# Kernel optimization log

Measured on AMD Instinct MI355X. Metric: run time of the kernel, lower is better.

Reference implementation:

```python
import jax, jax.numpy as jnp
import numpy as np

NH, DH, DHR = 16, 128, 64  # heads, head dim, decoupled rope dim
ROPE_BASE = 10000.0

def _rope(x):
    # x: (B, L, H, Dr) with Dr even; interleaved-pair RoPE (torchtune style)
    B, L, H, Dr = x.shape
    pos = jnp.arange(L, dtype=jnp.float32)
    inv_freq = 1.0 / (ROPE_BASE ** (jnp.arange(0, Dr, 2, dtype=jnp.float32) / Dr))
    ang = pos[:, None] * inv_freq[None, :]          # (L, Dr/2)
    cos = jnp.cos(ang)[None, :, None, :].astype(x.dtype)
    sin = jnp.sin(ang)[None, :, None, :].astype(x.dtype)
    x1, x2 = x[..., 0::2], x[..., 1::2]
    out = jnp.stack([x1 * cos - x2 * sin, x1 * sin + x2 * cos], axis=-1)
    return out.reshape(B, L, H, Dr)

def setup_inputs() -> dict:
    key = jax.random.key(0)
    ks = jax.random.split(key, 9)
    s = 0.02
    return {
        'x':     jax.random.normal(ks[0], (2, 2048, 2048), jnp.float32),
        'W_DKV': jax.random.normal(ks[1], (2048, 682), jnp.float32) * s,
        'W_UK':  jax.random.normal(ks[2], (682, 2048), jnp.float32) * s,
        'W_UV':  jax.random.normal(ks[3], (682, 2048), jnp.float32) * s,
        'W_KR':  jax.random.normal(ks[4], (2048, 64), jnp.float32) * s,
        'W_DQ':  jax.random.normal(ks[5], (2048, 682), jnp.float32) * s,
        'W_UQ':  jax.random.normal(ks[6], (682, 2048), jnp.float32) * s,
        'W_QR':  jax.random.normal(ks[7], (682, 1024), jnp.float32) * s,
        'W_O':   jax.random.normal(ks[8], (2048, 2048), jnp.float32) * s,
    }

def reference(x, W_DKV, W_UK, W_UV, W_KR, W_DQ, W_UQ, W_QR, W_O):
    B, L, D = x.shape
    # --- KV path ---
    c_KV = x @ W_DKV                                   # (B, L, dc)
    k_C = (c_KV @ W_UK).reshape(B, L, NH, DH)          # content keys
    k_R = _rope((x @ W_KR).reshape(B, L, 1, DHR))      # shared rope key head
    k_R = jnp.broadcast_to(k_R, (B, L, NH, DHR))
    k = jnp.concatenate([k_C, k_R], axis=-1)           # (B, L, NH, DH+DHR)
    v = (c_KV @ W_UV).reshape(B, L, NH, DH)
    # --- Q path ---
    c_Q = x @ W_DQ                                     # (B, L, dc')
    q_C = (c_Q @ W_UQ).reshape(B, L, NH, DH)
    q_R = _rope((c_Q @ W_QR).reshape(B, L, NH, DHR))
    q = jnp.concatenate([q_C, q_R], axis=-1)           # (B, L, NH, DH+DHR)
    # --- attention (causal) ---
    scale = 1.0 / jnp.sqrt(jnp.float32(DH + DHR))
    scores = jnp.einsum('blhd,bmhd->bhlm', q, k) * scale
    causal = jnp.tril(jnp.ones((L, L), dtype=bool))
    scores = jnp.where(causal[None, None], scores, jnp.finfo(scores.dtype).min)
    attn = jax.nn.softmax(scores, axis=-1)
    o = jnp.einsum('bhlm,bmhd->blhd', attn, v).reshape(B, L, NH * DH)
    return o @ W_O
```

## Files before the change

kernel.cpp:

```cpp
#include <hip/hip_runtime.h>
#include <stdint.h>

typedef __attribute__((ext_vector_type(8))) __bf16 bf16x8;
typedef __attribute__((ext_vector_type(4))) float f32x4;

#define DEVI static __device__ __forceinline__

DEVI uint16_t f2b(float f) {
  uint32_t u = __float_as_uint(f);
  u += 0x7FFFu + ((u >> 16) & 1u);
  return (uint16_t)(u >> 16);
}
DEVI float b2f(uint16_t b) { return __uint_as_float(((uint32_t)b) << 16); }

DEVI void gl_lds16(const void* g, void* l) {
  __builtin_amdgcn_global_load_lds((const __attribute__((address_space(1))) void*)g,
                                   (__attribute__((address_space(3))) void*)l, 16, 0, 0);
}

DEVI f32x4 mfma16(bf16x8 a, bf16x8 b, f32x4 c) {
  return __builtin_amdgcn_mfma_f32_16x16x32_bf16(a, b, c, 0, 0, 0);
}

#define BARX asm volatile("s_barrier" ::: "memory")
#define WLG0 asm volatile("s_waitcnt lgkmcnt(0)" ::: "memory")
#define WV4 asm volatile("s_waitcnt vmcnt(4)" ::: "memory")
#define PRIO1 __builtin_amdgcn_s_setprio(1)
#define PRIO0 __builtin_amdgcn_s_setprio(0)

static constexpr size_t OFF_XB = 0;
static constexpr size_t OFF_WD = 8388608;
static constexpr size_t OFF_WUKV = OFF_WD + 3670016;
static constexpr size_t OFF_WUQR = OFF_WUKV + 3145728;
static constexpr size_t OFF_WO = OFF_WUQR + 2359296;
static constexpr size_t OFF_CD = OFF_WO + 4194304;
static constexpr size_t OFF_CUKV = OFF_CD + 7340032;
static constexpr size_t OFF_CUQR = OFF_CUKV + 16777216;
static constexpr size_t OFF_VT = OFF_CUQR + 12582912;

__global__ void pre_kernel(const float* __restrict__ x, const float* __restrict__ Wdkv,
                           const float* __restrict__ Wuk, const float* __restrict__ Wuv,
                           const float* __restrict__ Wkr, const float* __restrict__ Wdq,
                           const float* __restrict__ Wuq, const float* __restrict__ Wqr,
                           const float* __restrict__ Wo, uint16_t* __restrict__ ws) {
  const int bid = blockIdx.x;
  const int t = threadIdx.x;
  if (bid >= 3264) {
    int id = (bid - 3264) * 256 + t;
    float4 v = ((const float4*)x)[id];
    uint16_t o[4] = {f2b(v.x), f2b(v.y), f2b(v.z), f2b(v.w)};
    *(uint64_t*)&ws[OFF_XB + (size_t)id * 4] = *(uint64_t*)o;
    return;
  }
  const float* W;
  uint16_t* Wt;
  int Kw, Nw, Kp, nx, rb;
  if (bid < 384) {
    W = Wdkv; Wt = ws + OFF_WD; Kw = 2048; Nw = 682; Kp = 2048; nx = 12; rb = bid;
  } else if (bid < 768) {
    W = Wdq; Wt = ws + OFF_WD + (size_t)768 * 2048; Kw = 2048; Nw = 682; Kp = 2048; nx = 12; rb = bid - 384;
  } else if (bid < 896) {
    W = Wkr; Wt = ws + OFF_WD + (size_t)1536 * 2048; Kw = 2048; Nw = 64; Kp = 2048; nx = 4; rb = bid - 768;
  } else if (bid < 1280) {
    W = Wuk; Wt = ws + OFF_WUKV; Kw = 682; Nw = 2048; Kp = 768; nx = 32; rb = bid - 896;
  } else if (bid < 1664) {
    W = Wuv; Wt = ws + OFF_WUKV + (size_t)2048 * 768; Kw = 682; Nw = 2048; Kp = 768; nx = 32; rb = bid - 1280;
  } else if (bid < 2048) {
    W = Wuq; Wt = ws + OFF_WUQR; Kw = 682; Nw = 2048; Kp = 768; nx = 32; rb = bid - 1664;
  } else if (bid < 2240) {
    W = Wqr; Wt = ws + OFF_WUQR + (size_t)2048 * 768; Kw = 682; Nw = 1024; Kp = 768; nx = 16; rb = bid - 2048;
  } else {
    W = Wo; Wt = ws + OFF_WO; Kw = 2048; Nw = 2048; Kp = 2048; nx = 32; rb = bid - 2240;
  }
  const int n0 = (rb % nx) * 64, k0 = (rb / nx) * 64;
  __shared__ uint16_t T[64][72];
#pragma unroll
  for (int p = 0; p < 2; ++p) {
    int r = p * 32 + (t >> 3);
    int c0 = (t & 7) * 8;
    int gr = k0 + r;
#pragma unroll
    for (int e = 0; e < 8; ++e) {
      int gc = n0 + c0 + e;
      float v = (gr < Kw && gc < Nw) ? W[(size_t)gr * Nw + gc] : 0.f;
      T[c0 + e][r] = f2b(v);
    }
  }
  __syncthreads();
#pragma unroll
  for (int p = 0; p < 2; ++p) {
    int dr = p * 32 + (t >> 3);
    int mc = (t & 7) * 8;
    uint16_t tmp[8];
#pragma unroll
    for (int e = 0; e < 8; ++e) tmp[e] = T[dr][mc + e];
    *(uint64_t*)&Wt[(size_t)(n0 + dr) * Kp + k0 + mc] = ((uint64_t*)tmp)[0];
    *(uint64_t*)&Wt[(size_t)(n0 + dr) * Kp + k0 + mc + 4] = ((uint64_t*)tmp)[1];
  }
}

template <int BM, bool F32OUT>
__global__ __launch_bounds__(512, 2) void gemm8(const uint16_t* __restrict__ A, int lda,
                                                const uint16_t* __restrict__ Bt,
                                                void* __restrict__ Cv, int ldc, int K) {
  constexpr int MF = BM / 32;
  constexpr int MH = MF / 2;
  constexpr int AL = BM / 128;
  constexpr int ABYTES = BM * 128;
  __shared__ char lds[2 * BM * 128 + 2 * 256 * 128];
  char* const LB = lds + 2 * ABYTES;
  const int tid = threadIdx.x;
  const int lane = tid & 63;
  const int lr = lane & 15, lgb = (lane >> 4) * 16;
  const int wid = tid >> 6;
  const int g = wid >> 2;
  const int wc = (wid & 3) * 64;
  const int rA0 = g * (BM / 2) + lr;
  const int rB0 = wc + lr;
  const size_t row0 = (size_t)blockIdx.y * BM, col0 = (size_t)blockIdx.x * 256;
  const char* Agb = (const char*)(A + row0 * lda);
  const char* Btb = (const char*)(Bt + col0 * K);
  const size_t ldab = (size_t)lda * 2;
  const size_t ldbb = (size_t)K * 2;
  const int nk = K >> 6;
  const int ni = nk >> 1;

  f32x4 acc[MF][4] = {};
  bf16x8 aF[MH][2], bF[4][2];

  auto stageA = [&](int kt, int buf, int hf) {
#pragma unroll
    for (int j = 0; j < AL; ++j) {
      int c = j * 512 + tid;
      int cl = c ^ (((c >> 5) & 1) << 1);
      int row = hf * (BM / 2) + (cl >> 3);
      gl_lds16(Agb + (size_t)row * ldab + (size_t)kt * 128 + (cl & 7) * 16,
               lds + buf * ABYTES + hf * (ABYTES / 2) + (j * 512 + (tid & 0x1C0)) * 16);
    }
  };
  auto stageB = [&](int kt, int buf, int hf) {
#pragma unroll
    for (int j = 0; j < 2; ++j) {
      int c = j * 512 + tid;
      int cl = c ^ (((c >> 5) & 1) << 1);
      int row = hf * 128 + (cl >> 3);
      gl_lds16(Btb + (size_t)row * ldbb + (size_t)kt * 128 + (cl & 7) * 16,
               LB + buf * 32768 + hf * 16384 + (j * 512 + (tid & 0x1C0)) * 16);
    }
  };
  auto ldAm = [&](int buf, int mb) {
#pragma unroll
    for (int m = 0; m < MH; ++m) {
      int r = rA0 + (mb + m) * 16;
      int ro = r * 128;
      int sw = ((r >> 2) & 1) << 5;
#pragma unroll
      for (int kk = 0; kk < 2; ++kk)
        aF[m][kk] = *(const bf16x8*)(lds + buf * ABYTES + ((ro + kk * 64 + lgb) ^ sw));
    }
  };
  auto ldBn = [&](int buf, int nb) {
#pragma unroll
    for (int n = 0; n < 2; ++n) {
      int r = rB0 + (nb + n) * 16;
      int ro = r * 128;
      int sw = ((r >> 2) & 1) << 5;
#pragma unroll
      for (int kk = 0; kk < 2; ++kk)
        bF[nb + n][kk] = *(const bf16x8*)(LB + buf * 32768 + ((ro + kk * 64 + lgb) ^ sw));
    }
  };
  auto mmac = [&](int mb, int nb) {
#pragma unroll
    for (int m = 0; m < MH; ++m)
#pragma unroll
      for (int n = 0; n < 2; ++n)
#pragma unroll
        for (int kk = 0; kk < 2; ++kk)
          acc[mb + m][nb + n] = mfma16(aF[m][kk], bF[nb + n][kk], acc[mb + m][nb + n]);
  };

  stageA(0, 0, 0); stageA(0, 0, 1); stageB(0, 0, 0); stageB(0, 0, 1);
  stageB(1, 1, 0); stageB(1, 1, 1);
  WV4; BARX;

  for (int i = 0; i < ni; ++i) {
    const int t1 = 2 * i + 1;
    const int tn = (2 * i + 2 < nk) ? 2 * i + 2 : nk - 1;
    const int tn1 = (2 * i + 3 < nk) ? 2 * i + 3 : nk - 1;
    ldAm(0, 0); ldBn(0, 0); stageA(t1, 1, 0);
    BARX; WLG0; PRIO1; mmac(0, 0); PRIO0; BARX;
    ldBn(0, 2); stageA(t1, 1, 1);
    BARX; WLG0; PRIO1; mmac(0, 2); PRIO0; BARX;
    ldAm(0, MH); stageB(tn, 0, 0);
    BARX; WLG0; PRIO1; mmac(MH, 0); PRIO0; BARX;
    stageB(tn, 0, 1);
    BARX; PRIO1; mmac(MH, 2); PRIO0; WV4; BARX;
    ldAm(1, 0); ldBn(1, 0); stageA(tn, 0, 0);
    BARX; WLG0; PRIO1; mmac(0, 0); PRIO0; BARX;
    ldBn(1, 2); stageA(tn, 0, 1);
    BARX; WLG0; PRIO1; mmac(0, 2); PRIO0; BARX;
    ldAm(1, MH); stageB(tn1, 1, 0);
    BARX; WLG0; PRIO1; mmac(MH, 0); PRIO0; BARX;
    stageB(tn1, 1, 1);
    BARX; PRIO1; mmac(MH, 2); PRIO0; WV4; BARX;
  }
  asm volatile("s_waitcnt vmcnt(0)" ::: "memory");

#pragma unroll
  for (int m = 0; m < MF; ++m)
#pragma unroll
    for (int n = 0; n < 4; ++n)
#pragma unroll
      for (int j = 0; j < 4; ++j) {
        size_t row = row0 + g * (BM / 2) + m * 16 + (lane >> 4) * 4 + j;
        size_t col = col0 + wc + n * 16 + lr;
        if (F32OUT)
          ((float*)Cv)[row * ldc + col] = acc[m][n][j];
        else
          ((uint16_t*)Cv)[row * ldc + col] = f2b(acc[m][n][j]);
      }
}

template <bool F32OUT>
__global__ __launch_bounds__(512, 2) void gemm4p(const uint16_t* __restrict__ A, int lda,
                                                 const uint16_t* __restrict__ Bt,
                                                 void* __restrict__ Cv, int ldc, int K) {
  constexpr int ABYTES = 128 * 128;
  __shared__ char lds[2 * ABYTES + 2 * 32768];
  char* const LB = lds + 2 * ABYTES;
  const int tid = threadIdx.x;
  const int lane = tid & 63;
  const int lr = lane & 15, lgb = (lane >> 4) * 16;
  const int wid = tid >> 6;
  const int g = wid >> 2;
  const int wc = (wid & 3) * 64;
  const int rA0 = g * 64 + lr;
  const int rB0 = wc + lr;
  const size_t row0 = (size_t)blockIdx.y * 128, col0 = (size_t)blockIdx.x * 256;
  const char* Agb = (const char*)(A + row0 * lda);
  const char* Btb = (const char*)(Bt + col0 * K);
  const size_t ldab = (size_t)lda * 2;
  const size_t ldbb = (size_t)K * 2;
  const int nk = K >> 6;
  const int ni = nk >> 1;

  f32x4 acc[4][4] = {};
  bf16x8 aF[2][2], bF[4][2];

  auto stageA = [&](int kt, int buf) {
#pragma unroll
    for (int j = 0; j < 2; ++j) {
      int c = j * 512 + tid;
      int cl = c ^ (((c >> 5) & 1) << 1);
      gl_lds16(Agb + (size_t)(cl >> 3) * ldab + (size_t)kt * 128 + (cl & 7) * 16,
               lds + buf * ABYTES + (j * 512 + (tid & 0x1C0)) * 16);
    }
  };
  auto stageBfull = [&](int kt, int buf) {
#pragma unroll
    for (int j = 0; j < 4; ++j) {
      int c = j * 512 + tid;
      int cl = c ^ (((c >> 5) & 1) << 1);
      gl_lds16(Btb + (size_t)(cl >> 3) * ldbb + (size_t)kt * 128 + (cl & 7) * 16,
               LB + buf * 32768 + (j * 512 + (tid & 0x1C0)) * 16);
    }
  };
  auto ldAm = [&](int buf, int mb) {
#pragma unroll
    for (int m = 0; m < 2; ++m) {
      int r = rA0 + (mb + m) * 16;
      int ro = r * 128;
      int sw = ((r >> 2) & 1) << 5;
#pragma unroll
      for (int kk = 0; kk < 2; ++kk)
        aF[m][kk] = *(const bf16x8*)(lds + buf * ABYTES + ((ro + kk * 64 + lgb) ^ sw));
    }
  };
  auto ldBn4 = [&](int buf) {
#pragma unroll
    for (int n = 0; n < 4; ++n) {
      int r = rB0 + n * 16;
      int ro = r * 128;
      int sw = ((r >> 2) & 1) << 5;
#pragma unroll
      for (int kk = 0; kk < 2; ++kk)
        bF[n][kk] = *(const bf16x8*)(LB + buf * 32768 + ((ro + kk * 64 + lgb) ^ sw));
    }
  };
  auto mmac16 = [&](int mb) {
#pragma unroll
    for (int m = 0; m < 2; ++m)
#pragma unroll
      for (int n = 0; n < 4; ++n)
#pragma unroll
        for (int kk = 0; kk < 2; ++kk)
          acc[mb + m][n] = mfma16(aF[m][kk], bF[n][kk], acc[mb + m][n]);
  };

  stageA(0, 0); stageBfull(0, 0); stageBfull(1, 1);
  WV4; BARX;

  for (int i = 0; i < ni; ++i) {
    const int t1 = 2 * i + 1;
    const int t2 = (2 * i + 2 < nk) ? 2 * i + 2 : nk - 1;
    const int t3 = (2 * i + 3 < nk) ? 2 * i + 3 : nk - 1;
    ldAm(0, 0); ldBn4(0); stageA(t1, 1);
    BARX; WLG0; PRIO1; mmac16(0); PRIO0; BARX;
    ldAm(0, 2); stageBfull(t2, 0);
    BARX; WLG0; PRIO1; mmac16(2); PRIO0; WV4; BARX;
    ldAm(1, 0); ldBn4(1); stageA(t2, 0);
    BARX; WLG0; PRIO1; mmac16(0); PRIO0; BARX;
    ldAm(1, 2); stageBfull(t3, 1);
    BARX; WLG0; PRIO1; mmac16(2); PRIO0; WV4; BARX;
  }
  asm volatile("s_waitcnt vmcnt(0)" ::: "memory");

#pragma unroll
  for (int m = 0; m < 4; ++m)
#pragma unroll
    for (int n = 0; n < 4; ++n)
#pragma unroll
      for (int j = 0; j < 4; ++j) {
        size_t row = row0 + g * 64 + m * 16 + (lane >> 4) * 4 + j;
        size_t col = col0 + wc + n * 16 + lr;
        if (F32OUT)
          ((float*)Cv)[row * ldc + col] = acc[m][n][j];
        else
          ((uint16_t*)Cv)[row * ldc + col] = f2b(acc[m][n][j]);
      }
}

__global__ void misc_kernel(uint16_t* __restrict__ cd, uint16_t* __restrict__ cuqr,
                            const uint16_t* __restrict__ cukv, uint16_t* __restrict__ vt) {
  const int bid = blockIdx.x;
  const int t = threadIdx.x;
  if (bid < 512) {
    int id = bid * 256 + t;
    int row = id >> 5, i = id & 31;
    int pos = row & 2047;
    float invf = exp2f(-13.287712379549449f * (float)i / 32.f);
    float ang = (float)pos * invf;
    float s, c;
    sincosf(ang, &s, &c);
    size_t base = (size_t)row * 1792 + 1536 + 2 * i;
    float x1 = b2f(cd[base]), x2 = b2f(cd[base + 1]);
    cd[base] = f2b(x1 * c - x2 * s);
    cd[base + 1] = f2b(x1 * s + x2 * c);
    return;
  }
  if (bid < 8704) {
    int id = (bid - 512) * 256 + t;
    int row = id >> 9;
    int rem = id & 511;
    int h = rem >> 5, i = rem & 31;
    int pos = row & 2047;
    float invf = exp2f(-13.287712379549449f * (float)i / 32.f);
    float ang = (float)pos * invf;
    float s, c;
    sincosf(ang, &s, &c);
    size_t base = (size_t)row * 3072 + 2048 + h * 64 + 2 * i;
    float x1 = b2f(cuqr[base]), x2 = b2f(cuqr[base + 1]);
    cuqr[base] = f2b(x1 * c - x2 * s);
    cuqr[base + 1] = f2b(x1 * s + x2 * c);
    return;
  }
  const int idx = bid - 8704;
  const int mt = idx & 31, dt = (idx >> 5) & 1, bh = idx >> 6;
  const int b = bh >> 4, h = bh & 15;
  const int m0 = mt * 64, d0 = dt * 64;
  __shared__ uint16_t T[64][72];
#pragma unroll
  for (int p = 0; p < 2; ++p) {
    int r = p * 32 + (t >> 3), c8 = (t & 7) * 8;
    const uint16_t* s = &cukv[((size_t)(b * 2048 + m0 + r)) * 4096 + 2048 + h * 128 + d0 + c8];
    uint16_t tmp[8];
    ((uint64_t*)tmp)[0] = ((const uint64_t*)s)[0];
    ((uint64_t*)tmp)[1] = ((const uint64_t*)s)[1];
#pragma unroll
    for (int e = 0; e < 8; ++e) T[c8 + e][r] = tmp[e];
  }
  __syncthreads();
#pragma unroll
  for (int p = 0; p < 2; ++p) {
    int dr = p * 32 + (t >> 3), mc = (t & 7) * 8;
    uint16_t tmp[8];
#pragma unroll
    for (int e = 0; e < 8; ++e) tmp[e] = T[dr][mc + e];
    uint16_t* dstp = &vt[((size_t)(bh * 128 + d0 + dr)) * 2048 + m0 + mc];
    ((uint64_t*)dstp)[0] = ((uint64_t*)tmp)[0];
    ((uint64_t*)dstp)[1] = ((uint64_t*)tmp)[1];
  }
}

__global__ __launch_bounds__(512, 2) void attn_kernel(const uint16_t* __restrict__ cuqr,
                                                      const uint16_t* __restrict__ cukv,
                                                      const uint16_t* __restrict__ cd,
                                                      const uint16_t* __restrict__ vt,
                                                      uint16_t* __restrict__ obuf) {
  __shared__ uint16_t Ks[2][64 * 192];
  __shared__ uint16_t Vs[2][128 * 64];
  __shared__ uint16_t Ps[8 * 16 * 64];
  const int tid = threadIdx.x;
  const int wid = tid >> 6, lane = tid & 63;
  const int lr = lane & 15, lg = lane >> 4;
  const int bid = blockIdx.x;
  const int wg = (bid & 7) * 32 + (bid >> 3);
  const int pairi = wg & 7;
  const int bh = wg >> 3;
  const int b = bh >> 4, h = bh & 15;
  const float sc2 = 0.07216878364870323f * 1.4426950408889634f;

  const char* Kcb = (const char*)cukv + (size_t)b * 2048 * 8192 + h * 256;
  const char* Krb = (const char*)cd + (size_t)b * 2048 * 3584 + 3072;
  const char* Vb = (const char*)vt + (size_t)bh * 524288;
  char* const Ks0 = (char*)Ks[0];
  char* const Vs0 = (char*)Vs[0];
  char* PwB = (char*)(Ps + wid * 1024);

  const char* kbase[3];
  size_t kstep[3];
  int klds[3];
#pragma unroll
  for (int i = 0; i < 3; ++i) {
    int c = i * 512 + tid;
    int r = c / 24, c16 = c % 24;
    klds[i] = r * 384 + ((c16 * 16) ^ ((r & 7) << 4));
    if (c16 < 16) {
      kbase[i] = Kcb + (size_t)r * 8192 + c16 * 16;
      kstep[i] = (size_t)64 * 8192;
    } else {
      kbase[i] = Krb + (size_t)r * 3584 + (c16 - 16) * 16;
      kstep[i] = (size_t)64 * 3584;
    }
  }
  const char* vbase[2];
  int vlds[2];
#pragma unroll
  for (int i = 0; i < 2; ++i) {
    int c = i * 512 + tid;
    int d = c >> 3, c16 = c & 7;
    vlds[i] = d * 128 + ((c16 * 16) ^ ((d & 7) << 4));
    vbase[i] = Vb + (size_t)d * 4096 + c16 * 16;
  }

  for (int ph = 0; ph < 2; ++ph) {
    const int qt = ph ? (15 - pairi) : pairi;
    const int q0 = qt * 128;
    const int nt = 2 * (qt + 1);
    const int qrow = q0 + wid * 16 + lr;
    bf16x8 qf[6];
    {
      const char* Qcp = (const char*)cuqr + (size_t)(b * 2048 + qrow) * 6144 + h * 256 + lg * 16;
      const char* Qrp =
          (const char*)cuqr + (size_t)(b * 2048 + qrow) * 6144 + 4096 + h * 128 + lg * 16;
#pragma unroll
      for (int kb = 0; kb < 4; ++kb) qf[kb] = *(const bf16x8*)(Qcp + kb * 64);
#pragma unroll
      for (int kb = 0; kb < 2; ++kb) qf[4 + kb] = *(const bf16x8*)(Qrp + kb * 64);
    }
    f32x4 o[8] = {};
    float mrun[4], lrun[4];
#pragma unroll
    for (int j = 0; j < 4; ++j) { mrun[j] = -INFINITY; lrun[j] = 0.f; }

    const char* kp[3];
    const char* vp[2];
    bf16x8 kreg[3], vreg[2];
#pragma unroll
    for (int i = 0; i < 3; ++i) kp[i] = kbase[i];
#pragma unroll
    for (int i = 0; i < 2; ++i) vp[i] = vbase[i];
#pragma unroll
    for (int i = 0; i < 3; ++i) { kreg[i] = *(const bf16x8*)kp[i]; kp[i] += kstep[i]; }
#pragma unroll
    for (int i = 0; i < 2; ++i) { vreg[i] = *(const bf16x8*)vp[i]; vp[i] += 128; }
#pragma unroll
    for (int i = 0; i < 3; ++i) *(bf16x8*)(Ks0 + klds[i]) = kreg[i];
#pragma unroll
    for (int i = 0; i < 2; ++i) *(bf16x8*)(Vs0 + vlds[i]) = vreg[i];
    __syncthreads();

    for (int t = 0; t < nt; ++t) {
      const bool more = (t + 1 < nt);
      if (more) {
#pragma unroll
        for (int i = 0; i < 3; ++i) { kreg[i] = *(const bf16x8*)kp[i]; kp[i] += kstep[i]; }
#pragma unroll
        for (int i = 0; i < 2; ++i) { vreg[i] = *(const bf16x8*)vp[i]; vp[i] += 128; }
      }
      const int cb = t & 1;
      const char* KsB = Ks0 + cb * 24576;
      const char* VsB = Vs0 + cb * 16384;
      if (t * 64 <= q0 + wid * 16 + 15) {
        f32x4 s[4] = {};
        __builtin_amdgcn_s_setprio(1);
#pragma unroll
        for (int n = 0; n < 4; ++n) {
          int r = n * 16 + lr;
          const char* kptr = KsB + r * 384;
          int sw = (r & 7) << 4;
#pragma unroll
          for (int kb = 0; kb < 6; ++kb)
            s[n] = mfma16(qf[kb], *(const bf16x8*)(kptr + ((kb * 64 + lg * 16) ^ sw)), s[n]);
        }
        __builtin_amdgcn_s_setprio(0);
        if (t * 64 + 63 > q0 + wid * 16) {
#pragma unroll
          for (int n = 0; n < 4; ++n)
#pragma unroll
            for (int j = 0; j < 4; ++j)
              if (t * 64 + n * 16 + lr > q0 + wid * 16 + lg * 4 + j) s[n][j] = -INFINITY;
        }
        float pm[4];
#pragma unroll
        for (int j = 0; j < 4; ++j) {
          float v = fmaxf(fmaxf(s[0][j], s[1][j]), fmaxf(s[2][j], s[3][j]));
          v = fmaxf(v, __shfl_xor(v, 1));
          v = fmaxf(v, __shfl_xor(v, 2));
          v = fmaxf(v, __shfl_xor(v, 4));
          v = fmaxf(v, __shfl_xor(v, 8));
          pm[j] = v;
        }
        bool exceed = false;
#pragma unroll
        for (int j = 0; j < 4; ++j) exceed |= (pm[j] > mrun[j] + 76.8f);
        if (__any(exceed)) {
          float alpha[4];
#pragma unroll
          for (int j = 0; j < 4; ++j) {
            float mn = fmaxf(mrun[j], pm[j]);
            alpha[j] = exp2f((mrun[j] - mn) * sc2);
            mrun[j] = mn;
            lrun[j] *= alpha[j];
          }
#pragma unroll
          for (int n2 = 0; n2 < 8; ++n2)
#pragma unroll
            for (int j = 0; j < 4; ++j) o[n2][j] *= alpha[j];
        }
        float rs[4] = {0.f, 0.f, 0.f, 0.f};
#pragma unroll
        for (int n = 0; n < 4; ++n)
#pragma unroll
          for (int j = 0; j < 4; ++j) {
            float p = exp2f((s[n][j] - mrun[j]) * sc2);
            rs[j] += p;
            int row = lg * 4 + j;
            *(uint16_t*)(PwB + row * 128 + ((((n * 16 + lr)) * 2) ^ ((row & 7) << 4))) = f2b(p);
          }
#pragma unroll
        for (int j = 0; j < 4; ++j) lrun[j] += rs[j];
        __builtin_amdgcn_s_setprio(1);
#pragma unroll
        for (int kb2 = 0; kb2 < 2; ++kb2) {
          bf16x8 pa = *(const bf16x8*)(PwB + lr * 128 + ((kb2 * 64 + lg * 16) ^ ((lr & 7) << 4)));
#pragma unroll
          for (int n2 = 0; n2 < 8; ++n2) {
            int vr = n2 * 16 + lr;
            o[n2] = mfma16(
                pa, *(const bf16x8*)(VsB + vr * 128 + ((kb2 * 64 + lg * 16) ^ ((vr & 7) << 4))),
                o[n2]);
          }
        }
        __builtin_amdgcn_s_setprio(0);
      }
      if (more) {
        char* KsN = Ks0 + (cb ^ 1) * 24576;
        char* VsN = Vs0 + (cb ^ 1) * 16384;
#pragma unroll
        for (int i = 0; i < 3; ++i) *(bf16x8*)(KsN + klds[i]) = kreg[i];
#pragma unroll
        for (int i = 0; i < 2; ++i) *(bf16x8*)(VsN + vlds[i]) = vreg[i];
      }
      __syncthreads();
    }
#pragma unroll
    for (int j = 0; j < 4; ++j) {
      float v = lrun[j];
      v += __shfl_xor(v, 1);
      v += __shfl_xor(v, 2);
      v += __shfl_xor(v, 4);
      v += __shfl_xor(v, 8);
      lrun[j] = v;
    }
    float inv[4];
#pragma unroll
    for (int j = 0; j < 4; ++j) inv[j] = 1.f / lrun[j];
#pragma unroll
    for (int n2 = 0; n2 < 8; ++n2)
#pragma unroll
      for (int j = 0; j < 4; ++j) {
        size_t row = (size_t)b * 2048 + q0 + wid * 16 + lg * 4 + j;
        size_t col = (size_t)h * 128 + n2 * 16 + lr;
        obuf[row * 2048 + col] = f2b(o[n2][j] * inv[j]);
      }
  }
}

extern "C" void kernel_launch(void* const* d_in, const int* in_sizes, int n_in,
                              void* d_out, int out_size, void* d_ws, size_t ws_size,
                              hipStream_t stream) {
  (void)in_sizes; (void)n_in; (void)out_size; (void)ws_size;
  const float* x = (const float*)d_in[0];
  const float* Wdkv = (const float*)d_in[1];
  const float* Wuk = (const float*)d_in[2];
  const float* Wuv = (const float*)d_in[3];
  const float* Wkr = (const float*)d_in[4];
  const float* Wdq = (const float*)d_in[5];
  const float* Wuq = (const float*)d_in[6];
  const float* Wqr = (const float*)d_in[7];
  const float* Wo = (const float*)d_in[8];
  uint16_t* ws = (uint16_t*)d_ws;

  uint16_t* xb = ws + OFF_XB;
  uint16_t* obuf = ws + OFF_XB;
  uint16_t* wd = ws + OFF_WD;
  uint16_t* wukv = ws + OFF_WUKV;
  uint16_t* wuqr = ws + OFF_WUQR;
  uint16_t* wo = ws + OFF_WO;
  uint16_t* cd = ws + OFF_CD;
  uint16_t* cukv = ws + OFF_CUKV;
  uint16_t* cuqr = ws + OFF_CUQR;
  uint16_t* vtb = ws + OFF_VT;

  pre_kernel<<<11456, 256, 0, stream>>>(x, Wdkv, Wuk, Wuv, Wkr, Wdq, Wuq, Wqr, Wo, ws);
  gemm4p<false><<<dim3(7, 32), 512, 0, stream>>>(xb, 2048, wd, cd, 1792, 2048);
  gemm8<256, false><<<dim3(16, 16), 512, 0, stream>>>(cd, 1792, wukv, cukv, 4096, 768);
  gemm8<256, false><<<dim3(12, 16), 512, 0, stream>>>(cd + 768, 1792, wuqr, cuqr, 3072, 768);
  misc_kernel<<<10752, 256, 0, stream>>>(cd, cuqr, cukv, vtb);
  attn_kernel<<<256, 512, 0, stream>>>(cuqr, cukv, cd, vtb, obuf);
  gemm4p<true><<<dim3(8, 32), 512, 0, stream>>>(obuf, 2048, wo, d_out, 2048, 2048);
}
```

Before: 267.0 us.

## Merge up-projection GEMMs into one dual launch with fused query RoPE epilogue

Replaces the two separate up-projection GEMM launches with a single dual-problem kernel that chooses its operands by block index. The query RoPE rotation moves into that kernel's epilogue using lane shuffles, which removes the matching elementwise pass from the misc kernel. The gemm4p kernel is replaced by gemm8<128> for the down-projection and output GEMMs. This saves launches, a read-modify-write pass over the RoPE columns, and tail imbalance between the two GEMMs. In exchange, RoPE is now applied to fp32 accumulators before bf16 rounding, and the epilogue gains sincos work.

```diff
diff --git a/kernel.cpp b/kernel.cpp
--- a/kernel.cpp
+++ b/kernel.cpp
@@ -222,12 +222,17 @@
       }
 }
 
-template <bool F32OUT>
-__global__ __launch_bounds__(512, 2) void gemm4p(const uint16_t* __restrict__ A, int lda,
-                                                 const uint16_t* __restrict__ Bt,
-                                                 void* __restrict__ Cv, int ldc, int K) {
-  constexpr int ABYTES = 128 * 128;
-  __shared__ char lds[2 * ABYTES + 2 * 32768];
+__global__ __launch_bounds__(512, 2) void gemm8dual(const uint16_t* __restrict__ A1,
+                                                    const uint16_t* __restrict__ A2, int lda,
+                                                    const uint16_t* __restrict__ Bt1,
+                                                    const uint16_t* __restrict__ Bt2,
+                                                    uint16_t* __restrict__ C1, int ldc1,
+                                                    uint16_t* __restrict__ C2, int ldc2,
+                                                    int K) {
+  constexpr int BM = 256;
+  constexpr int MF = 8, MH = 4, AL = 2;
+  constexpr int ABYTES = BM * 128;
+  __shared__ char lds[2 * BM * 128 + 2 * 256 * 128];
   char* const LB = lds + 2 * ABYTES;
   const int tid = threadIdx.x;
   const int lane = tid & 63;
@@ -235,9 +240,16 @@
   const int wid = tid >> 6;
   const int g = wid >> 2;
   const int wc = (wid & 3) * 64;
-  const int rA0 = g * 64 + lr;
+  const int rA0 = g * (BM / 2) + lr;
   const int rB0 = wc + lr;
-  const size_t row0 = (size_t)blockIdx.y * 128, col0 = (size_t)blockIdx.x * 256;
+  const bool second = blockIdx.x >= 16;
+  const int xl = second ? blockIdx.x - 16 : blockIdx.x;
+  const uint16_t* A = second ? A2 : A1;
+  const uint16_t* Bt = second ? Bt2 : Bt1;
+  uint16_t* Cv = second ? C2 : C1;
+  const int ldc = second ? ldc2 : ldc1;
+  const bool doRope = second && (xl >= 8);
+  const size_t row0 = (size_t)blockIdx.y * BM, col0 = (size_t)xl * 256;
   const char* Agb = (const char*)(A + row0 * lda);
   const char* Btb = (const char*)(Bt + col0 * K);
   const size_t ldab = (size_t)lda * 2;
@@ -245,30 +257,32 @@
   const int nk = K >> 6;
   const int ni = nk >> 1;
 
-  f32x4 acc[4][4] = {};
-  bf16x8 aF[2][2], bF[4][2];
-
-  auto stageA = [&](int kt, int buf) {
+  f32x4 acc[MF][4] = {};
+  bf16x8 aF[MH][2], bF[4][2];
+
+  auto stageA = [&](int kt, int buf, int hf) {
+#pragma unroll
+    for (int j = 0; j < AL; ++j) {
+      int c = j * 512 + tid;
+      int cl = c ^ (((c >> 5) & 1) << 1);
+      int row = hf * (BM / 2) + (cl >> 3);
+      gl_lds16(Agb + (size_t)row * ldab + (size_t)kt * 128 + (cl & 7) * 16,
+               lds + buf * ABYTES + hf * (ABYTES / 2) + (j * 512 + (tid & 0x1C0)) * 16);
+    }
+  };
+  auto stageB = [&](int kt, int buf, int hf) {
 #pragma unroll
     for (int j = 0; j < 2; ++j) {
       int c = j * 512 + tid;
       int cl = c ^ (((c >> 5) & 1) << 1);
-      gl_lds16(Agb + (size_t)(cl >> 3) * ldab + (size_t)kt * 128 + (cl & 7) * 16,
-               lds + buf * ABYTES + (j * 512 + (tid & 0x1C0)) * 16);
-    }
-  };
-  auto stageBfull = [&](int kt, int buf) {
-#pragma unroll
-    for (int j = 0; j < 4; ++j) {
-      int c = j * 512 + tid;
-      int cl = c ^ (((c >> 5) & 1) << 1);
-      gl_lds16(Btb + (size_t)(cl >> 3) * ldbb + (size_t)kt * 128 + (cl & 7) * 16,
-               LB + buf * 32768 + (j * 512 + (tid & 0x1C0)) * 16);
+      int row = hf * 128 + (cl >> 3);
+      gl_lds16(Btb + (size_t)row * ldbb + (size_t)kt * 128 + (cl & 7) * 16,
+               LB + buf * 32768 + hf * 16384 + (j * 512 + (tid & 0x1C0)) * 16);
     }
   };
   auto ldAm = [&](int buf, int mb) {
 #pragma unroll
-    for (int m = 0; m < 2; ++m) {
+    for (int m = 0; m < MH; ++m) {
       int r = rA0 + (mb + m) * 16;
       int ro = r * 128;
       int sw = ((r >> 2) & 1) << 5;
@@ -277,62 +291,87 @@
         aF[m][kk] = *(const bf16x8*)(lds + buf * ABYTES + ((ro + kk * 64 + lgb) ^ sw));
     }
   };
-  auto ldBn4 = [&](int buf) {
-#pragma unroll
-    for (int n = 0; n < 4; ++n) {
-      int r = rB0 + n * 16;
+  auto ldBn = [&](int buf, int nb) {
+#pragma unroll
+    for (int n = 0; n < 2; ++n) {
+      int r = rB0 + (nb + n) * 16;
       int ro = r * 128;
       int sw = ((r >> 2) & 1) << 5;
 #pragma unroll
       for (int kk = 0; kk < 2; ++kk)
-        bF[n][kk] = *(const bf16x8*)(LB + buf * 32768 + ((ro + kk * 64 + lgb) ^ sw));
-    }
-  };
-  auto mmac16 = [&](int mb) {
-#pragma unroll
-    for (int m = 0; m < 2; ++m)
-#pragma unroll
-      for (int n = 0; n < 4; ++n)
+        bF[nb + n][kk] = *(const bf16x8*)(LB + buf * 32768 + ((ro + kk * 64 + lgb) ^ sw));
+    }
+  };
+  auto mmac = [&](int mb, int nb) {
+#pragma unroll
+    for (int m = 0; m < MH; ++m)
+#pragma unroll
+      for (int n = 0; n < 2; ++n)
 #pragma unroll
         for (int kk = 0; kk < 2; ++kk)
-          acc[mb + m][n] = mfma16(aF[m][kk], bF[n][kk], acc[mb + m][n]);
-  };
-
-  stageA(0, 0); stageBfull(0, 0); stageBfull(1, 1);
+          acc[mb + m][nb + n] = mfma16(aF[m][kk], bF[nb + n][kk], acc[mb + m][nb + n]);
+  };
+
+  stageA(0, 0, 0); stageA(0, 0, 1); stageB(0, 0, 0); stageB(0, 0, 1);
+  stageB(1, 1, 0); stageB(1, 1, 1);
   WV4; BARX;
 
   for (int i = 0; i < ni; ++i) {
     const int t1 = 2 * i + 1;
-    const int t2 = (2 * i + 2 < nk) ? 2 * i + 2 : nk - 1;
-    const int t3 = (2 * i + 3 < nk) ? 2 * i + 3 : nk - 1;
-    ldAm(0, 0); ldBn4(0); stageA(t1, 1);
-    BARX; WLG0; PRIO1; mmac16(0); PRIO0; BARX;
-    ldAm(0, 2); stageBfull(t2, 0);
-    BARX; WLG0; PRIO1; mmac16(2); PRIO0; WV4; BARX;
-    ldAm(1, 0); ldBn4(1); stageA(t2, 0);
-    BARX; WLG0; PRIO1; mmac16(0); PRIO0; BARX;
-    ldAm(1, 2); stageBfull(t3, 1);
-    BARX; WLG0; PRIO1; mmac16(2); PRIO0; WV4; BARX;
+    const int tn = (2 * i + 2 < nk) ? 2 * i + 2 : nk - 1;
+    const int tn1 = (2 * i + 3 < nk) ? 2 * i + 3 : nk - 1;
+    ldAm(0, 0); ldBn(0, 0); stageA(t1, 1, 0);
+    BARX; WLG0; PRIO1; mmac(0, 0); PRIO0; BARX;
+    ldBn(0, 2); stageA(t1, 1, 1);
+    BARX; WLG0; PRIO1; mmac(0, 2); PRIO0; BARX;
+    ldAm(0, MH); stageB(tn, 0, 0);
+    BARX; WLG0; PRIO1; mmac(MH, 0); PRIO0; BARX;
+    stageB(tn, 0, 1);
+    BARX; PRIO1; mmac(MH, 2); PRIO0; WV4; BARX;
+    ldAm(1, 0); ldBn(1, 0); stageA(tn, 0, 0);
+    BARX; WLG0; PRIO1; mmac(0, 0); PRIO0; BARX;
+    ldBn(1, 2); stageA(tn, 0, 1);
+    BARX; WLG0; PRIO1; mmac(0, 2); PRIO0; BARX;
+    ldAm(1, MH); stageB(tn1, 1, 0);
+    BARX; WLG0; PRIO1; mmac(MH, 0); PRIO0; BARX;
+    stageB(tn1, 1, 1);
+    BARX; PRIO1; mmac(MH, 2); PRIO0; WV4; BARX;
   }
   asm volatile("s_waitcnt vmcnt(0)" ::: "memory");
 
-#pragma unroll
-  for (int m = 0; m < 4; ++m)
+  if (doRope) {
+#pragma unroll
+    for (int m = 0; m < MF; ++m)
+#pragma unroll
+      for (int n = 0; n < 4; ++n) {
+        const int c64 = n * 16 + lr;
+        const float invf = exp2f(-13.287712379549449f * (float)(c64 >> 1) / 32.f);
+#pragma unroll
+        for (int j = 0; j < 4; ++j) {
+          int row = (int)(row0 + g * (BM / 2) + m * 16 + (lane >> 4) * 4 + j);
+          float ang = (float)(row & 2047) * invf;
+          float sv, cv;
+          sincosf(ang, &sv, &cv);
+          float own = acc[m][n][j];
+          float part = __shfl_xor(own, 1);
+          acc[m][n][j] = ((lr & 1) == 0) ? (own * cv - part * sv) : (part * sv + own * cv);
+        }
+      }
+  }
+#pragma unroll
+  for (int m = 0; m < MF; ++m)
 #pragma unroll
     for (int n = 0; n < 4; ++n)
 #pragma unroll
       for (int j = 0; j < 4; ++j) {
-        size_t row = row0 + g * 64 + m * 16 + (lane >> 4) * 4 + j;
+        size_t row = row0 + g * (BM / 2) + m * 16 + (lane >> 4) * 4 + j;
         size_t col = col0 + wc + n * 16 + lr;
-        if (F32OUT)
-          ((float*)Cv)[row * ldc + col] = acc[m][n][j];
-        else
-          ((uint16_t*)Cv)[row * ldc + col] = f2b(acc[m][n][j]);
+        Cv[row * ldc + col] = f2b(acc[m][n][j]);
       }
 }
 
-__global__ void misc_kernel(uint16_t* __restrict__ cd, uint16_t* __restrict__ cuqr,
-                            const uint16_t* __restrict__ cukv, uint16_t* __restrict__ vt) {
+__global__ void misc_kernel(uint16_t* __restrict__ cd, const uint16_t* __restrict__ cukv,
+                            uint16_t* __restrict__ vt) {
   const int bid = blockIdx.x;
   const int t = threadIdx.x;
   if (bid < 512) {
@@ -349,23 +388,7 @@
     cd[base + 1] = f2b(x1 * s + x2 * c);
     return;
   }
-  if (bid < 8704) {
-    int id = (bid - 512) * 256 + t;
-    int row = id >> 9;
-    int rem = id & 511;
-    int h = rem >> 5, i = rem & 31;
-    int pos = row & 2047;
-    float invf = exp2f(-13.287712379549449f * (float)i / 32.f);
-    float ang = (float)pos * invf;
-    float s, c;
-    sincosf(ang, &s, &c);
-    size_t base = (size_t)row * 3072 + 2048 + h * 64 + 2 * i;
-    float x1 = b2f(cuqr[base]), x2 = b2f(cuqr[base + 1]);
-    cuqr[base] = f2b(x1 * c - x2 * s);
-    cuqr[base + 1] = f2b(x1 * s + x2 * c);
-    return;
-  }
-  const int idx = bid - 8704;
+  const int idx = bid - 512;
   const int mt = idx & 31, dt = (idx >> 5) & 1, bh = idx >> 6;
   const int b = bh >> 4, h = bh & 15;
   const int m0 = mt * 64, d0 = dt * 64;
@@ -625,10 +648,10 @@
   uint16_t* vtb = ws + OFF_VT;
 
   pre_kernel<<<11456, 256, 0, stream>>>(x, Wdkv, Wuk, Wuv, Wkr, Wdq, Wuq, Wqr, Wo, ws);
-  gemm4p<false><<<dim3(7, 32), 512, 0, stream>>>(xb, 2048, wd, cd, 1792, 2048);
-  gemm8<256, false><<<dim3(16, 16), 512, 0, stream>>>(cd, 1792, wukv, cukv, 4096, 768);
-  gemm8<256, false><<<dim3(12, 16), 512, 0, stream>>>(cd + 768, 1792, wuqr, cuqr, 3072, 768);
-  misc_kernel<<<10752, 256, 0, stream>>>(cd, cuqr, cukv, vtb);
+  gemm8<128, false><<<dim3(7, 32), 512, 0, stream>>>(xb, 2048, wd, cd, 1792, 2048);
+  gemm8dual<<<dim3(28, 16), 512, 0, stream>>>(cd, cd + 768, 1792, wukv, wuqr,
+                                              cukv, 4096, cuqr, 3072, 768);
+  misc_kernel<<<2560, 256, 0, stream>>>(cd, cukv, vtb);
   attn_kernel<<<256, 512, 0, stream>>>(cuqr, cukv, cd, vtb, obuf);
-  gemm4p<true><<<dim3(8, 32), 512, 0, stream>>>(obuf, 2048, wo, d_out, 2048, 2048);
-}
+  gemm8<128, true><<<dim3(8, 32), 512, 0, stream>>>(obuf, 2048, wo, d_out, 2048, 2048);
+}
```

Result: slower. 343.3 us (+28.6%).
